# Kernel optimization log

Hardware: AMD Instinct MI355X
Metric: run time of the kernel (lower is better)

## Reference

```python
import jax, jax.numpy as jnp
import numpy as np

V = 50000
D = 128
EF = 16
E = 800000
LN_EPS = 1e-5


def setup_inputs() -> dict:
    key = jax.random.key(0)
    ks = jax.random.split(key, 9)
    h = jax.random.normal(ks[0], (V, D), dtype=jnp.float32)
    edge_index = jax.random.randint(ks[1], (2, E), 0, V, dtype=jnp.int64)
    edge_attr = jax.random.normal(ks[2], (E, EF), dtype=jnp.float32)
    # msg_mlp = Linear(D+EF, D) -> ReLU -> Dropout(0) -> Linear(D, D)
    s1 = 1.0 / np.sqrt(D + EF)
    s2 = 1.0 / np.sqrt(D)
    W1 = jax.random.uniform(ks[3], (D + EF, D), minval=-s1, maxval=s1, dtype=jnp.float32)
    b1 = jax.random.uniform(ks[4], (D,), minval=-s1, maxval=s1, dtype=jnp.float32)
    W2 = jax.random.uniform(ks[5], (D, D), minval=-s2, maxval=s2, dtype=jnp.float32)
    b2 = jax.random.uniform(ks[6], (D,), minval=-s2, maxval=s2, dtype=jnp.float32)
    gamma = jnp.ones((D,), dtype=jnp.float32)
    beta = jnp.zeros((D,), dtype=jnp.float32)
    return {"h": h, "edge_index": edge_index, "edge_attr": edge_attr,
            "W1": W1, "b1": b1, "W2": W2, "b2": b2,
            "gamma": gamma, "beta": beta}


def _layer_norm(x, gamma, beta):
    mu = jnp.mean(x, axis=-1, keepdims=True)
    var = jnp.mean(jnp.square(x - mu), axis=-1, keepdims=True)
    return (x - mu) * jax.lax.rsqrt(var + LN_EPS) * gamma + beta


def reference(h, edge_index, edge_attr, W1, b1, W2, b2, gamma, beta):
    src, dst = edge_index[0], edge_index[1]
    # gather source node features, concat edge features: [E, D+EF]
    x = jnp.concatenate([h[src], edge_attr], axis=-1)
    # per-edge message MLP (dropout p=0 -> identity)
    msg = jax.nn.relu(x @ W1 + b1) @ W2 + b2  # [E, D]
    # scatter-add messages to destinations
    agg = jax.ops.segment_sum(msg, dst, num_segments=V)  # [V, D]
    # count initialized to ones BEFORE scatter_add -> denominator = 1 + in_degree
    deg = jax.ops.segment_sum(jnp.ones((E,), dtype=h.dtype), dst, num_segments=V)
    count = (1.0 + deg)[:, None]  # [V, 1]
    return _layer_norm(h + agg / count, gamma, beta)
```

## Files before the change

kernel.cpp:

```cpp
#include <hip/hip_runtime.h>
#include <hip/hip_bf16.h>

#define V 50000
#define D 128
#define EF 16
#define E_EDGES 800000
#define NT 12500
#define USTR 136
#define XESTR 40
#define CSTR 136
#define NSCAN 196
#define EGRID 1024
#define UGRID 782

typedef __attribute__((ext_vector_type(8))) __bf16 bf16x8;
typedef __attribute__((ext_vector_type(4))) float f32x4;

__device__ inline unsigned short f2bf(float f) {
    unsigned u = __float_as_uint(f);
    u += 0x7FFF + ((u >> 16) & 1);
    return (unsigned short)(u >> 16);
}
__device__ inline unsigned pack2(float a, float b) {
    return (unsigned)f2bf(a) | ((unsigned)f2bf(b) << 16);
}
__device__ inline float bf2f(unsigned short u) {
    return __uint_as_float((unsigned)u << 16);
}

__global__ __launch_bounds__(256)
void setup_kernel(const int* __restrict__ ei, int* __restrict__ cnt,
                  float* __restrict__ agg,
                  const float* __restrict__ W1, const float* __restrict__ W2,
                  unsigned short* __restrict__ W1p, unsigned short* __restrict__ W2p) {
    int idx = blockIdx.x * 256 + threadIdx.x;
    *(float4*)(agg + ((size_t)idx << 2)) = (float4){0.f, 0.f, 0.f, 0.f};
    if (idx < E_EDGES) atomicAdd(&cnt[ei[E_EDGES + idx]], 1);
    if (idx < 5 * 128 * 32) {
        int kb = idx >> 12, rem = idx & 4095;
        int n = rem >> 5, kk = rem & 31;
        int k = kb * 32 + kk;
        W1p[idx] = f2bf((k < D + EF) ? W1[k * D + n] : 0.0f);
    }
    if (idx < 4 * 128 * 32) {
        int kb = idx >> 12, rem = idx & 4095;
        int n = rem >> 5, kk = rem & 31;
        W2p[idx] = f2bf(W2[(kb * 32 + kk) * D + n]);
    }
}

__global__ __launch_bounds__(256)
void u_gemm_kernel(const float* __restrict__ h,
                   const unsigned short* __restrict__ W1p,
                   unsigned short* __restrict__ U) {
    __shared__ __align__(16) unsigned short Hs[64 * USTR];
    const int tid  = threadIdx.x;
    const int lane = tid & 63;
    const int wave = tid >> 6;
    const int nlo  = lane & 15;
    const int kq   = lane >> 4;
    const int er   = tid >> 4;
    const int ec   = tid & 15;
    const int gbase = blockIdx.x << 6;

    bf16x8 B1[4][2];
    #pragma unroll
    for (int t = 0; t < 2; ++t) {
        int n = wave * 32 + t * 16 + nlo;
        #pragma unroll
        for (int kb = 0; kb < 4; ++kb)
            B1[kb][t] = *(const bf16x8*)(W1p + ((kb << 7) + n) * 32 + (kq << 3));
    }

    #pragma unroll
    for (int m = 0; m < 4; ++m) {
        int row = er + m * 16;
        int grow = gbase + row;
        unsigned* o = (unsigned*)(Hs + row * USTR + (ec << 3));
        if (grow < V) {
            const float4* p = (const float4*)(h + (size_t)grow * D + (ec << 3));
            float4 v0 = p[0], v1 = p[1];
            o[0] = pack2(v0.x, v0.y); o[1] = pack2(v0.z, v0.w);
            o[2] = pack2(v1.x, v1.y); o[3] = pack2(v1.z, v1.w);
        } else {
            o[0] = 0u; o[1] = 0u; o[2] = 0u; o[3] = 0u;
        }
    }
    __syncthreads();

    f32x4 acc[4][2];
    #pragma unroll
    for (int mt = 0; mt < 4; ++mt)
        #pragma unroll
        for (int t = 0; t < 2; ++t)
            acc[mt][t] = (f32x4){0.f, 0.f, 0.f, 0.f};

    #pragma unroll
    for (int kb = 0; kb < 4; ++kb) {
        bf16x8 A[4];
        int ko = kb * 32 + (kq << 3);
        #pragma unroll
        for (int mt = 0; mt < 4; ++mt)
            A[mt] = *(const bf16x8*)(Hs + (mt * 16 + nlo) * USTR + ko);
        #pragma unroll
        for (int mt = 0; mt < 4; ++mt)
            #pragma unroll
            for (int t = 0; t < 2; ++t)
                acc[mt][t] = __builtin_amdgcn_mfma_f32_16x16x32_bf16(A[mt], B1[kb][t], acc[mt][t], 0, 0, 0);
    }

    #pragma unroll
    for (int mt = 0; mt < 4; ++mt)
        #pragma unroll
        for (int t = 0; t < 2; ++t)
            #pragma unroll
            for (int r = 0; r < 4; ++r) {
                int row = mt * 16 + (kq << 2) + r;
                int grow = gbase + row;
                int col = wave * 32 + t * 16 + nlo;
                if (grow < V)
                    U[(size_t)grow * D + col] = f2bf(acc[mt][t][r]);
            }
}

__device__ inline int block_excl_scan(int x, int t, int* ws) {
    int lane = t & 63, w = t >> 6;
    int inc = x;
    #pragma unroll
    for (int off = 1; off < 64; off <<= 1) {
        int y = __shfl_up(inc, off);
        if (lane >= off) inc += y;
    }
    if (lane == 63) ws[w] = inc;
    __syncthreads();
    if (t == 0) {
        int r = 0;
        #pragma unroll
        for (int i = 0; i < 4; ++i) { int c = ws[i]; ws[i] = r; r += c; }
    }
    __syncthreads();
    return inc - x + ws[w];
}

__global__ __launch_bounds__(256)
void scan1_kernel(const int* __restrict__ cnt, int* __restrict__ cursor,
                  int* __restrict__ bsum) {
    __shared__ int ws[4];
    __shared__ int tot;
    int t = threadIdx.x;
    int i = blockIdx.x * 256 + t;
    int x = (i < V) ? cnt[i] : 0;
    int ex = block_excl_scan(x, t, ws);
    if (i < V) cursor[i] = ex;
    if (t == 255) tot = ex + x;
    __syncthreads();
    if (t == 0) bsum[blockIdx.x] = tot;
}

__global__ __launch_bounds__(256)
void scatter_kernel(const int* __restrict__ ei, int* __restrict__ cursor,
                    const int* __restrict__ bsum,
                    int* __restrict__ srcs, int* __restrict__ dsts,
                    int* __restrict__ eidx) {
    __shared__ int ws[4];
    __shared__ int sboff[NSCAN];
    int t = threadIdx.x;
    int x = (t < NSCAN) ? bsum[t] : 0;
    int ex = block_excl_scan(x, t, ws);
    if (t < NSCAN) sboff[t] = ex;
    __syncthreads();
    int e = blockIdx.x * 256 + t;
    int d = ei[E_EDGES + e];
    int pos = atomicAdd(&cursor[d], 1) + sboff[d >> 8];
    srcs[pos] = ei[e];
    dsts[pos] = d;
    eidx[pos] = e;
}

__global__ __launch_bounds__(256, 4)
void edge_kernel(const unsigned short* __restrict__ U,
                 const float* __restrict__ ea,
                 const int* __restrict__ srcs, const int* __restrict__ dsts,
                 const int* __restrict__ eidx,
                 const unsigned short* __restrict__ W1p, const unsigned short* __restrict__ W2p,
                 const float* __restrict__ b1, const float* __restrict__ b2,
                 float* __restrict__ agg) {
    __shared__ __align__(16) unsigned short Us[64 * USTR];
    __shared__ __align__(16) _Float16 Cs[64 * CSTR];
    __shared__ __align__(16) unsigned short Xe[64 * XESTR];
    __shared__ int sDst[2][64];

    const int tid  = threadIdx.x;
    const int lane = tid & 63;
    const int wave = tid >> 6;
    const int nlo  = lane & 15;
    const int kq   = lane >> 4;
    const int er   = tid >> 4;
    const int ec   = tid & 15;
    const int ee   = tid >> 2;
    const int eq   = tid & 3;

    bf16x8 B1e[2], B2[4][2];
    float b1v[2], b2v[2];
    #pragma unroll
    for (int t = 0; t < 2; ++t) {
        int n = wave * 32 + t * 16 + nlo;
        b1v[t] = b1[n];
        b2v[t] = b2[n];
        B1e[t] = *(const bf16x8*)(W1p + ((4 << 7) + n) * 32 + (kq << 3));
        #pragma unroll
        for (int kb = 0; kb < 4; ++kb)
            B2[kb][t] = *(const bf16x8*)(W2p + ((kb << 7) + n) * 32 + (kq << 3));
    }

    {
        unsigned* xz = (unsigned*)Xe;
        int i0 = tid, i1 = tid + 256;
        xz[(i0 >> 3) * (XESTR / 2) + 8 + (i0 & 7)] = 0u;
        xz[(i1 >> 3) * (XESTR / 2) + 8 + (i1 & 7)] = 0u;
    }

    const int base0 = blockIdx.x << 6;
    int a0 = srcs[base0 + er];
    int a1 = srcs[base0 + er + 16];
    int a2 = srcs[base0 + er + 32];
    int a3 = srcs[base0 + er + 48];
    int aev = eidx[base0 + ee];
    int ddcur = dsts[base0 + lane];
    bf16x8 pf0 = *(const bf16x8*)(U + (size_t)a0 * D + (ec << 3));
    bf16x8 pf1 = *(const bf16x8*)(U + (size_t)a1 * D + (ec << 3));
    bf16x8 pf2 = *(const bf16x8*)(U + (size_t)a2 * D + (ec << 3));
    bf16x8 pf3 = *(const bf16x8*)(U + (size_t)a3 * D + (ec << 3));
    float4 pfe = *(const float4*)(ea + (size_t)aev * EF + (eq << 2));

    int n1 = blockIdx.x + EGRID;
    int nb1 = (n1 < NT ? n1 : blockIdx.x) << 6;
    int i1s0 = srcs[nb1 + er];
    int i1s1 = srcs[nb1 + er + 16];
    int i1s2 = srcs[nb1 + er + 32];
    int i1s3 = srcs[nb1 + er + 48];
    int i1e  = eidx[nb1 + ee];
    int i1d  = dsts[nb1 + lane];

    int buf = 0;
    for (int tile = blockIdx.x; tile < NT; tile += EGRID) {
        if (tid < 64) sDst[buf][tid] = ddcur;
        *(bf16x8*)(Us + er * USTR + (ec << 3))        = pf0;
        *(bf16x8*)(Us + (er + 16) * USTR + (ec << 3)) = pf1;
        *(bf16x8*)(Us + (er + 32) * USTR + (ec << 3)) = pf2;
        *(bf16x8*)(Us + (er + 48) * USTR + (ec << 3)) = pf3;
        {
            unsigned* xp = (unsigned*)Xe + ee * (XESTR / 2) + (eq << 1);
            xp[0] = pack2(pfe.x, pfe.y);
            xp[1] = pack2(pfe.z, pfe.w);
        }
        __syncthreads();

        f32x4 accE[4][2];
        #pragma unroll
        for (int mt = 0; mt < 4; ++mt)
            #pragma unroll
            for (int t = 0; t < 2; ++t)
                #pragma unroll
                for (int r = 0; r < 4; ++r)
                    accE[mt][t][r] = bf2f(Us[(mt * 16 + (kq << 2) + r) * USTR + wave * 32 + t * 16 + nlo]);
        {
            bf16x8 A[4];
            #pragma unroll
            for (int mt = 0; mt < 4; ++mt)
                A[mt] = *(const bf16x8*)(Xe + (mt * 16 + nlo) * XESTR + (kq << 3));
            #pragma unroll
            for (int mt = 0; mt < 4; ++mt)
                #pragma unroll
                for (int t = 0; t < 2; ++t)
                    accE[mt][t] = __builtin_amdgcn_mfma_f32_16x16x32_bf16(A[mt], B1e[t], accE[mt][t], 0, 0, 0);
        }

        #pragma unroll
        for (int mt = 0; mt < 4; ++mt)
            #pragma unroll
            for (int t = 0; t < 2; ++t)
                #pragma unroll
                for (int r = 0; r < 4; ++r) {
                    int row = mt * 16 + (kq << 2) + r;
                    int col = wave * 32 + t * 16 + nlo;
                    Us[row * USTR + col] = f2bf(fmaxf(accE[mt][t][r] + b1v[t], 0.0f));
                }
        __syncthreads();

        f32x4 acc2[4][2];
        #pragma unroll
        for (int mt = 0; mt < 4; ++mt)
            #pragma unroll
            for (int t = 0; t < 2; ++t)
                acc2[mt][t] = (f32x4){0.f, 0.f, 0.f, 0.f};

        #pragma unroll
        for (int kb = 0; kb < 4; ++kb) {
            bf16x8 A[4];
            int ko = kb * 32 + (kq << 3);
            #pragma unroll
            for (int mt = 0; mt < 4; ++mt)
                A[mt] = *(const bf16x8*)(Us + (mt * 16 + nlo) * USTR + ko);
            #pragma unroll
            for (int mt = 0; mt < 4; ++mt)
                #pragma unroll
                for (int t = 0; t < 2; ++t)
                    acc2[mt][t] = __builtin_amdgcn_mfma_f32_16x16x32_bf16(A[mt], B2[kb][t], acc2[mt][t], 0, 0, 0);
        }

        #pragma unroll
        for (int mt = 0; mt < 4; ++mt)
            #pragma unroll
            for (int t = 0; t < 2; ++t)
                #pragma unroll
                for (int r = 0; r < 4; ++r) {
                    int row = mt * 16 + (kq << 2) + r;
                    int col = wave * 32 + t * 16 + nlo;
                    Cs[row * CSTR + col] = (_Float16)(acc2[mt][t][r] + b2v[t]);
                }
        __syncthreads();

        int n2 = tile + 2 * EGRID;
        int nb2 = (n2 < NT ? n2 : tile) << 6;
        int i2s0 = srcs[nb2 + er];
        int i2s1 = srcs[nb2 + er + 16];
        int i2s2 = srcs[nb2 + er + 32];
        int i2s3 = srcs[nb2 + er + 48];
        int i2e  = eidx[nb2 + ee];
        int i2d  = dsts[nb2 + lane];

        bf16x8 q0 = *(const bf16x8*)(U + (size_t)i1s0 * D + (ec << 3));
        bf16x8 q1 = *(const bf16x8*)(U + (size_t)i1s1 * D + (ec << 3));
        bf16x8 q2 = *(const bf16x8*)(U + (size_t)i1s2 * D + (ec << 3));
        bf16x8 q3 = *(const bf16x8*)(U + (size_t)i1s3 * D + (ec << 3));
        float4 qe = *(const float4*)(ea + (size_t)i1e * EF + (eq << 2));
        int nextdd = i1d;

        {
            int col = tid & 127;
            int rbase = (tid >> 7) << 5;
            float sum = 0.f;
            int cur = sDst[buf][rbase];
            for (int i = 0; i < 32; ++i) {
                int d = sDst[buf][rbase + i];
                if (d != cur) {
                    atomicAdd(&agg[(size_t)cur * D + col], sum);
                    sum = 0.f;
                    cur = d;
                }
                sum += (float)Cs[(rbase + i) * CSTR + col];
            }
            atomicAdd(&agg[(size_t)cur * D + col], sum);
        }

        pf0 = q0; pf1 = q1; pf2 = q2; pf3 = q3; pfe = qe; ddcur = nextdd;
        i1s0 = i2s0; i1s1 = i2s1; i1s2 = i2s2; i1s3 = i2s3; i1e = i2e; i1d = i2d;
        buf ^= 1;
    }
}

__global__ __launch_bounds__(256)
void finalize_kernel(const float* __restrict__ h, const float* __restrict__ agg,
                     const int* __restrict__ cnt,
                     const float* __restrict__ gamma, const float* __restrict__ beta,
                     float* __restrict__ out) {
    int wave = threadIdx.x >> 6, lane = threadIdx.x & 63;
    int v = blockIdx.x * 4 + wave;
    if (v >= V) return;
    float inv = 1.0f / (1.0f + (float)cnt[v]);
    const float* hr = h + (size_t)v * D;
    const float* ar = agg + (size_t)v * D;
    float x0 = hr[lane]      + ar[lane]      * inv;
    float x1 = hr[lane + 64] + ar[lane + 64] * inv;
    float s = x0 + x1;
    #pragma unroll
    for (int m = 32; m; m >>= 1) s += __shfl_xor(s, m);
    float mu = s * (1.0f / 128.0f);
    float d0 = x0 - mu, d1 = x1 - mu;
    float vs = d0 * d0 + d1 * d1;
    #pragma unroll
    for (int m = 32; m; m >>= 1) vs += __shfl_xor(vs, m);
    float rs = rsqrtf(vs * (1.0f / 128.0f) + 1e-5f);
    out[(size_t)v * D + lane]      = d0 * rs * gamma[lane]      + beta[lane];
    out[(size_t)v * D + 64 + lane] = d1 * rs * gamma[lane + 64] + beta[lane + 64];
}

extern "C" void kernel_launch(void* const* d_in, const int* in_sizes, int n_in,
                              void* d_out, int out_size, void* d_ws, size_t ws_size,
                              hipStream_t stream) {
    const float* h     = (const float*)d_in[0];
    const int*   ei    = (const int*)d_in[1];
    const float* ea    = (const float*)d_in[2];
    const float* W1    = (const float*)d_in[3];
    const float* b1    = (const float*)d_in[4];
    const float* W2    = (const float*)d_in[5];
    const float* b2    = (const float*)d_in[6];
    const float* gamma = (const float*)d_in[7];
    const float* beta  = (const float*)d_in[8];
    float* out = (float*)d_out;

    char* ws = (char*)d_ws;
    float*          agg    = (float*)ws;
    int*            cnt    = (int*)(ws + 25600000);
    int*            cursor = (int*)(ws + 25800000);
    int*            bsum   = (int*)(ws + 26000000);
    int*            srcs   = (int*)(ws + 26000800);
    int*            dsts   = (int*)(ws + 29200800);
    int*            eidx   = (int*)(ws + 32400800);
    unsigned short* W1p    = (unsigned short*)(ws + 35600800);
    unsigned short* W2p    = (unsigned short*)(ws + 35641760);
    unsigned short* U      = (unsigned short*)(ws + 35674528);

    hipMemsetAsync(cnt, 0, 200000, stream);
    setup_kernel<<<6250, 256, 0, stream>>>(ei, cnt, agg, W1, W2, W1p, W2p);
    u_gemm_kernel<<<UGRID, 256, 0, stream>>>(h, W1p, U);
    scan1_kernel<<<NSCAN, 256, 0, stream>>>(cnt, cursor, bsum);
    scatter_kernel<<<3125, 256, 0, stream>>>(ei, cursor, bsum, srcs, dsts, eidx);
    edge_kernel<<<EGRID, 256, 0, stream>>>(U, ea, srcs, dsts, eidx, W1p, W2p, b1, b2, agg);
    finalize_kernel<<<12500, 256, 0, stream>>>(h, agg, cnt, gamma, beta, out);
}
```

Measured before the change: 322.3 us.

## Use 512-thread edge blocks with one 16-column MFMA slice per wave

The edge kernel now launches 512 threads (8 waves) per block instead of 256. Each wave owns a single 16-column output slice rather than two, which halves the per-thread accumulators, weight fragments and gather loads, and the launch bounds target 6 blocks per CU. The persistent grid drops from 1024 to 768 blocks, and each thread's segmented scatter-add covers 16 rows instead of 32, which may raise the number of atomics to agg. The aim is more waves in flight to hide gather latency, at the cost of smaller MFMA work per wave and more block-level synchronisation overhead.

```diff
diff --git a/kernel.cpp b/kernel.cpp
--- a/kernel.cpp
+++ b/kernel.cpp
@@ -10,7 +10,7 @@
 #define XESTR 40
 #define CSTR 136
 #define NSCAN 196
-#define EGRID 1024
+#define EGRID 768
 #define UGRID 782
 
 typedef __attribute__((ext_vector_type(8))) __bf16 bf16x8;
@@ -177,7 +177,7 @@
     eidx[pos] = e;
 }
 
-__global__ __launch_bounds__(256, 4)
+__global__ __launch_bounds__(512, 6)
 void edge_kernel(const unsigned short* __restrict__ U,
                  const float* __restrict__ ea,
                  const int* __restrict__ srcs, const int* __restrict__ dsts,
@@ -197,73 +197,54 @@
     const int kq   = lane >> 4;
     const int er   = tid >> 4;
     const int ec   = tid & 15;
-    const int ee   = tid >> 2;
-    const int eq   = tid & 3;
-
-    bf16x8 B1e[2], B2[4][2];
-    float b1v[2], b2v[2];
-    #pragma unroll
-    for (int t = 0; t < 2; ++t) {
-        int n = wave * 32 + t * 16 + nlo;
-        b1v[t] = b1[n];
-        b2v[t] = b2[n];
-        B1e[t] = *(const bf16x8*)(W1p + ((4 << 7) + n) * 32 + (kq << 3));
-        #pragma unroll
-        for (int kb = 0; kb < 4; ++kb)
-            B2[kb][t] = *(const bf16x8*)(W2p + ((kb << 7) + n) * 32 + (kq << 3));
-    }
+    const int ee   = tid >> 3;
+    const int eq   = tid & 7;
+
+    bf16x8 B1e, B2[4];
+    float b1v, b2v;
+    const int ncol = wave * 16 + nlo;
+    b1v = b1[ncol];
+    b2v = b2[ncol];
+    B1e = *(const bf16x8*)(W1p + ((4 << 7) + ncol) * 32 + (kq << 3));
+    #pragma unroll
+    for (int kb = 0; kb < 4; ++kb)
+        B2[kb] = *(const bf16x8*)(W2p + ((kb << 7) + ncol) * 32 + (kq << 3));
 
     {
         unsigned* xz = (unsigned*)Xe;
-        int i0 = tid, i1 = tid + 256;
-        xz[(i0 >> 3) * (XESTR / 2) + 8 + (i0 & 7)] = 0u;
-        xz[(i1 >> 3) * (XESTR / 2) + 8 + (i1 & 7)] = 0u;
+        xz[(tid >> 3) * (XESTR / 2) + 8 + (tid & 7)] = 0u;
     }
 
     const int base0 = blockIdx.x << 6;
     int a0 = srcs[base0 + er];
-    int a1 = srcs[base0 + er + 16];
-    int a2 = srcs[base0 + er + 32];
-    int a3 = srcs[base0 + er + 48];
+    int a1 = srcs[base0 + er + 32];
     int aev = eidx[base0 + ee];
-    int ddcur = dsts[base0 + lane];
+    int ddcur = dsts[base0 + (tid & 63)];
     bf16x8 pf0 = *(const bf16x8*)(U + (size_t)a0 * D + (ec << 3));
     bf16x8 pf1 = *(const bf16x8*)(U + (size_t)a1 * D + (ec << 3));
-    bf16x8 pf2 = *(const bf16x8*)(U + (size_t)a2 * D + (ec << 3));
-    bf16x8 pf3 = *(const bf16x8*)(U + (size_t)a3 * D + (ec << 3));
-    float4 pfe = *(const float4*)(ea + (size_t)aev * EF + (eq << 2));
+    float2 pfe = *(const float2*)(ea + (size_t)aev * EF + (eq << 1));
 
     int n1 = blockIdx.x + EGRID;
     int nb1 = (n1 < NT ? n1 : blockIdx.x) << 6;
     int i1s0 = srcs[nb1 + er];
-    int i1s1 = srcs[nb1 + er + 16];
-    int i1s2 = srcs[nb1 + er + 32];
-    int i1s3 = srcs[nb1 + er + 48];
+    int i1s1 = srcs[nb1 + er + 32];
     int i1e  = eidx[nb1 + ee];
-    int i1d  = dsts[nb1 + lane];
+    int i1d  = dsts[nb1 + (tid & 63)];
 
     int buf = 0;
     for (int tile = blockIdx.x; tile < NT; tile += EGRID) {
         if (tid < 64) sDst[buf][tid] = ddcur;
         *(bf16x8*)(Us + er * USTR + (ec << 3))        = pf0;
-        *(bf16x8*)(Us + (er + 16) * USTR + (ec << 3)) = pf1;
-        *(bf16x8*)(Us + (er + 32) * USTR + (ec << 3)) = pf2;
-        *(bf16x8*)(Us + (er + 48) * USTR + (ec << 3)) = pf3;
-        {
-            unsigned* xp = (unsigned*)Xe + ee * (XESTR / 2) + (eq << 1);
-            xp[0] = pack2(pfe.x, pfe.y);
-            xp[1] = pack2(pfe.z, pfe.w);
-        }
+        *(bf16x8*)(Us + (er + 32) * USTR + (ec << 3)) = pf1;
+        ((unsigned*)Xe)[ee * (XESTR / 2) + eq] = pack2(pfe.x, pfe.y);
         __syncthreads();
 
-        f32x4 accE[4][2];
-        #pragma unroll
-        for (int mt = 0; mt < 4; ++mt)
-            #pragma unroll
-            for (int t = 0; t < 2; ++t)
-                #pragma unroll
-                for (int r = 0; r < 4; ++r)
-                    accE[mt][t][r] = bf2f(Us[(mt * 16 + (kq << 2) + r) * USTR + wave * 32 + t * 16 + nlo]);
+        f32x4 accE[4];
+        #pragma unroll
+        for (int mt = 0; mt < 4; ++mt)
+            #pragma unroll
+            for (int r = 0; r < 4; ++r)
+                accE[mt][r] = bf2f(Us[(mt * 16 + (kq << 2) + r) * USTR + ncol]);
         {
             bf16x8 A[4];
             #pragma unroll
@@ -271,29 +252,22 @@
                 A[mt] = *(const bf16x8*)(Xe + (mt * 16 + nlo) * XESTR + (kq << 3));
             #pragma unroll
             for (int mt = 0; mt < 4; ++mt)
-                #pragma unroll
-                for (int t = 0; t < 2; ++t)
-                    accE[mt][t] = __builtin_amdgcn_mfma_f32_16x16x32_bf16(A[mt], B1e[t], accE[mt][t], 0, 0, 0);
+                accE[mt] = __builtin_amdgcn_mfma_f32_16x16x32_bf16(A[mt], B1e, accE[mt], 0, 0, 0);
         }
 
         #pragma unroll
         for (int mt = 0; mt < 4; ++mt)
             #pragma unroll
-            for (int t = 0; t < 2; ++t)
-                #pragma unroll
-                for (int r = 0; r < 4; ++r) {
-                    int row = mt * 16 + (kq << 2) + r;
-                    int col = wave * 32 + t * 16 + nlo;
-                    Us[row * USTR + col] = f2bf(fmaxf(accE[mt][t][r] + b1v[t], 0.0f));
-                }
+            for (int r = 0; r < 4; ++r) {
+                int row = mt * 16 + (kq << 2) + r;
+                Us[row * USTR + ncol] = f2bf(fmaxf(accE[mt][r] + b1v, 0.0f));
+            }
         __syncthreads();
 
-        f32x4 acc2[4][2];
-        #pragma unroll
-        for (int mt = 0; mt < 4; ++mt)
-            #pragma unroll
-            for (int t = 0; t < 2; ++t)
-                acc2[mt][t] = (f32x4){0.f, 0.f, 0.f, 0.f};
+        f32x4 acc2[4];
+        #pragma unroll
+        for (int mt = 0; mt < 4; ++mt)
+            acc2[mt] = (f32x4){0.f, 0.f, 0.f, 0.f};
 
         #pragma unroll
         for (int kb = 0; kb < 4; ++kb) {
@@ -304,45 +278,37 @@
                 A[mt] = *(const bf16x8*)(Us + (mt * 16 + nlo) * USTR + ko);
             #pragma unroll
             for (int mt = 0; mt < 4; ++mt)
-                #pragma unroll
-                for (int t = 0; t < 2; ++t)
-                    acc2[mt][t] = __builtin_amdgcn_mfma_f32_16x16x32_bf16(A[mt], B2[kb][t], acc2[mt][t], 0, 0, 0);
+                acc2[mt] = __builtin_amdgcn_mfma_f32_16x16x32_bf16(A[mt], B2[kb], acc2[mt], 0, 0, 0);
         }
 
         #pragma unroll
         for (int mt = 0; mt < 4; ++mt)
             #pragma unroll
-            for (int t = 0; t < 2; ++t)
-                #pragma unroll
-                for (int r = 0; r < 4; ++r) {
-                    int row = mt * 16 + (kq << 2) + r;
-                    int col = wave * 32 + t * 16 + nlo;
-                    Cs[row * CSTR + col] = (_Float16)(acc2[mt][t][r] + b2v[t]);
-                }
+            for (int r = 0; r < 4; ++r) {
+                int row = mt * 16 + (kq << 2) + r;
+                Cs[row * CSTR + ncol] = (_Float16)(acc2[mt][r] + b2v);
+            }
         __syncthreads();
 
         int n2 = tile + 2 * EGRID;
         int nb2 = (n2 < NT ? n2 : tile) << 6;
         int i2s0 = srcs[nb2 + er];
-        int i2s1 = srcs[nb2 + er + 16];
-        int i2s2 = srcs[nb2 + er + 32];
-        int i2s3 = srcs[nb2 + er + 48];
+        int i2s1 = srcs[nb2 + er + 32];
         int i2e  = eidx[nb2 + ee];
-        int i2d  = dsts[nb2 + lane];
+        int i2d  = dsts[nb2 + (tid & 63)];
 
         bf16x8 q0 = *(const bf16x8*)(U + (size_t)i1s0 * D + (ec << 3));
         bf16x8 q1 = *(const bf16x8*)(U + (size_t)i1s1 * D + (ec << 3));
-        bf16x8 q2 = *(const bf16x8*)(U + (size_t)i1s2 * D + (ec << 3));
-        bf16x8 q3 = *(const bf16x8*)(U + (size_t)i1s3 * D + (ec << 3));
-        float4 qe = *(const float4*)(ea + (size_t)i1e * EF + (eq << 2));
+        float2 qe = *(const float2*)(ea + (size_t)i1e * EF + (eq << 1));
         int nextdd = i1d;
 
         {
             int col = tid & 127;
-            int rbase = (tid >> 7) << 5;
+            int rbase = (tid >> 7) << 4;
             float sum = 0.f;
             int cur = sDst[buf][rbase];
-            for (int i = 0; i < 32; ++i) {
+            #pragma unroll 4
+            for (int i = 0; i < 16; ++i) {
                 int d = sDst[buf][rbase + i];
                 if (d != cur) {
                     atomicAdd(&agg[(size_t)cur * D + col], sum);
@@ -354,8 +320,8 @@
             atomicAdd(&agg[(size_t)cur * D + col], sum);
         }
 
-        pf0 = q0; pf1 = q1; pf2 = q2; pf3 = q3; pfe = qe; ddcur = nextdd;
-        i1s0 = i2s0; i1s1 = i2s1; i1s2 = i2s2; i1s3 = i2s3; i1e = i2e; i1d = i2d;
+        pf0 = q0; pf1 = q1; pfe = qe; ddcur = nextdd;
+        i1s0 = i2s0; i1s1 = i2s1; i1e = i2e; i1d = i2d;
         buf ^= 1;
     }
 }
@@ -417,6 +383,6 @@
     u_gemm_kernel<<<UGRID, 256, 0, stream>>>(h, W1p, U);
     scan1_kernel<<<NSCAN, 256, 0, stream>>>(cnt, cursor, bsum);
     scatter_kernel<<<3125, 256, 0, stream>>>(ei, cursor, bsum, srcs, dsts, eidx);
-    edge_kernel<<<EGRID, 256, 0, stream>>>(U, ea, srcs, dsts, eidx, W1p, W2p, b1, b2, agg);
+    edge_kernel<<<EGRID, 512, 0, stream>>>(U, ea, srcs, dsts, eidx, W1p, W2p, b1, b2, agg);
     finalize_kernel<<<12500, 256, 0, stream>>>(h, agg, cnt, gamma, beta, out);
 }
```

Measured after the change: 327.9 us. Within noise of the previous version (+1.7%).

## Transpose MFMA operands for vectorized LDS epilogues and float4 scatter reduction

Applied to the files above, without the earlier changes.

Swaps the A/B operands of the MFMA calls so each lane holds four consecutive output columns, which lets the accumulator init, the bias+ReLU writeback and the fp16 output store use 64-bit packed LDS accesses instead of scalar 16-bit ones. Bias loads become float4, conversions use hardware packed bf16/fp16 converts, and the segmented scatter reduction now walks 8 rows with 4 columns per thread. The reduction emits four scalar atomics per flush over shorter row segments, so atomic traffic to agg may rise. The fp16 packing uses round-toward-zero, which changes rounding slightly.

```diff
diff --git a/kernel.cpp b/kernel.cpp
--- a/kernel.cpp
+++ b/kernel.cpp
@@ -15,6 +15,8 @@
 
 typedef __attribute__((ext_vector_type(8))) __bf16 bf16x8;
 typedef __attribute__((ext_vector_type(4))) float f32x4;
+typedef __attribute__((ext_vector_type(2))) __fp16 fp16x2;
+typedef __attribute__((ext_vector_type(2))) _Float16 f16x2;
 
 __device__ inline unsigned short f2bf(float f) {
     unsigned u = __float_as_uint(f);
@@ -26,6 +28,16 @@
 }
 __device__ inline float bf2f(unsigned short u) {
     return __uint_as_float((unsigned)u << 16);
+}
+__device__ inline unsigned pkbf(float a, float b) {
+    union { __hip_bfloat162 h; unsigned u; } v;
+    v.h = __float22bfloat162_rn(make_float2(a, b));
+    return v.u;
+}
+__device__ inline unsigned pkf16(float a, float b) {
+    union { fp16x2 h; unsigned u; } v;
+    v.h = __builtin_amdgcn_cvt_pkrtz(a, b);
+    return v.u;
 }
 
 __global__ __launch_bounds__(256)
@@ -201,12 +213,12 @@
     const int eq   = tid & 3;
 
     bf16x8 B1e[2], B2[4][2];
-    float b1v[2], b2v[2];
+    float4 b1n[2], b2n[2];
     #pragma unroll
     for (int t = 0; t < 2; ++t) {
         int n = wave * 32 + t * 16 + nlo;
-        b1v[t] = b1[n];
-        b2v[t] = b2[n];
+        b1n[t] = *(const float4*)(b1 + wave * 32 + t * 16 + (kq << 2));
+        b2n[t] = *(const float4*)(b2 + wave * 32 + t * 16 + (kq << 2));
         B1e[t] = *(const bf16x8*)(W1p + ((4 << 7) + n) * 32 + (kq << 3));
         #pragma unroll
         for (int kb = 0; kb < 4; ++kb)
@@ -251,8 +263,8 @@
         *(bf16x8*)(Us + (er + 48) * USTR + (ec << 3)) = pf3;
         {
             unsigned* xp = (unsigned*)Xe + ee * (XESTR / 2) + (eq << 1);
-            xp[0] = pack2(pfe.x, pfe.y);
-            xp[1] = pack2(pfe.z, pfe.w);
+            xp[0] = pkbf(pfe.x, pfe.y);
+            xp[1] = pkbf(pfe.z, pfe.w);
         }
         __syncthreads();
 
@@ -260,32 +272,36 @@
         #pragma unroll
         for (int mt = 0; mt < 4; ++mt)
             #pragma unroll
-            for (int t = 0; t < 2; ++t)
-                #pragma unroll
-                for (int r = 0; r < 4; ++r)
-                    accE[mt][t][r] = bf2f(Us[(mt * 16 + (kq << 2) + r) * USTR + wave * 32 + t * 16 + nlo]);
+            for (int t = 0; t < 2; ++t) {
+                uint2 uu = *(const uint2*)(Us + (mt * 16 + nlo) * USTR + wave * 32 + t * 16 + (kq << 2));
+                accE[mt][t][0] = bf2f((unsigned short)uu.x);
+                accE[mt][t][1] = bf2f((unsigned short)(uu.x >> 16));
+                accE[mt][t][2] = bf2f((unsigned short)uu.y);
+                accE[mt][t][3] = bf2f((unsigned short)(uu.y >> 16));
+            }
         {
-            bf16x8 A[4];
+            bf16x8 Xf[4];
             #pragma unroll
             for (int mt = 0; mt < 4; ++mt)
-                A[mt] = *(const bf16x8*)(Xe + (mt * 16 + nlo) * XESTR + (kq << 3));
+                Xf[mt] = *(const bf16x8*)(Xe + (mt * 16 + nlo) * XESTR + (kq << 3));
             #pragma unroll
             for (int mt = 0; mt < 4; ++mt)
                 #pragma unroll
                 for (int t = 0; t < 2; ++t)
-                    accE[mt][t] = __builtin_amdgcn_mfma_f32_16x16x32_bf16(A[mt], B1e[t], accE[mt][t], 0, 0, 0);
+                    accE[mt][t] = __builtin_amdgcn_mfma_f32_16x16x32_bf16(B1e[t], Xf[mt], accE[mt][t], 0, 0, 0);
         }
 
         #pragma unroll
         for (int mt = 0; mt < 4; ++mt)
             #pragma unroll
-            for (int t = 0; t < 2; ++t)
-                #pragma unroll
-                for (int r = 0; r < 4; ++r) {
-                    int row = mt * 16 + (kq << 2) + r;
-                    int col = wave * 32 + t * 16 + nlo;
-                    Us[row * USTR + col] = f2bf(fmaxf(accE[mt][t][r] + b1v[t], 0.0f));
-                }
+            for (int t = 0; t < 2; ++t) {
+                uint2 yw;
+                yw.x = pkbf(fmaxf(accE[mt][t][0] + b1n[t].x, 0.0f),
+                            fmaxf(accE[mt][t][1] + b1n[t].y, 0.0f));
+                yw.y = pkbf(fmaxf(accE[mt][t][2] + b1n[t].z, 0.0f),
+                            fmaxf(accE[mt][t][3] + b1n[t].w, 0.0f));
+                *(uint2*)(Us + (mt * 16 + nlo) * USTR + wave * 32 + t * 16 + (kq << 2)) = yw;
+            }
         __syncthreads();
 
         f32x4 acc2[4][2];
@@ -297,28 +313,27 @@
 
         #pragma unroll
         for (int kb = 0; kb < 4; ++kb) {
-            bf16x8 A[4];
+            bf16x8 Yf[4];
             int ko = kb * 32 + (kq << 3);
             #pragma unroll
             for (int mt = 0; mt < 4; ++mt)
-                A[mt] = *(const bf16x8*)(Us + (mt * 16 + nlo) * USTR + ko);
+                Yf[mt] = *(const bf16x8*)(Us + (mt * 16 + nlo) * USTR + ko);
             #pragma unroll
             for (int mt = 0; mt < 4; ++mt)
                 #pragma unroll
                 for (int t = 0; t < 2; ++t)
-                    acc2[mt][t] = __builtin_amdgcn_mfma_f32_16x16x32_bf16(A[mt], B2[kb][t], acc2[mt][t], 0, 0, 0);
+                    acc2[mt][t] = __builtin_amdgcn_mfma_f32_16x16x32_bf16(B2[kb][t], Yf[mt], acc2[mt][t], 0, 0, 0);
         }
 
         #pragma unroll
         for (int mt = 0; mt < 4; ++mt)
             #pragma unroll
-            for (int t = 0; t < 2; ++t)
-                #pragma unroll
-                for (int r = 0; r < 4; ++r) {
-                    int row = mt * 16 + (kq << 2) + r;
-                    int col = wave * 32 + t * 16 + nlo;
-                    Cs[row * CSTR + col] = (_Float16)(acc2[mt][t][r] + b2v[t]);
-                }
+            for (int t = 0; t < 2; ++t) {
+                uint2 cw;
+                cw.x = pkf16(acc2[mt][t][0] + b2n[t].x, acc2[mt][t][1] + b2n[t].y);
+                cw.y = pkf16(acc2[mt][t][2] + b2n[t].z, acc2[mt][t][3] + b2n[t].w);
+                *(uint2*)((unsigned short*)Cs + (size_t)(mt * 16 + nlo) * CSTR + wave * 32 + t * 16 + (kq << 2)) = cw;
+            }
         __syncthreads();
 
         int n2 = tile + 2 * EGRID;
@@ -338,20 +353,30 @@
         int nextdd = i1d;
 
         {
-            int col = tid & 127;
-            int rbase = (tid >> 7) << 5;
-            float sum = 0.f;
-            int cur = sDst[buf][rbase];
-            for (int i = 0; i < 32; ++i) {
-                int d = sDst[buf][rbase + i];
+            int q = tid & 31;
+            int mb = (tid >> 5) << 3;
+            float4 sum = {0.f, 0.f, 0.f, 0.f};
+            int cur = sDst[buf][mb];
+            #pragma unroll
+            for (int i = 0; i < 8; ++i) {
+                int m = mb + i;
+                int d = sDst[buf][m];
                 if (d != cur) {
-                    atomicAdd(&agg[(size_t)cur * D + col], sum);
-                    sum = 0.f;
+                    float* ap = agg + (size_t)cur * D + (q << 2);
+                    atomicAdd(ap + 0, sum.x); atomicAdd(ap + 1, sum.y);
+                    atomicAdd(ap + 2, sum.z); atomicAdd(ap + 3, sum.w);
+                    sum = (float4){0.f, 0.f, 0.f, 0.f};
                     cur = d;
                 }
-                sum += (float)Cs[(rbase + i) * CSTR + col];
+                uint2 cr = *(const uint2*)((const unsigned short*)Cs + (size_t)m * CSTR + (q << 2));
+                union { unsigned u; f16x2 h; } c0, c1;
+                c0.u = cr.x; c1.u = cr.y;
+                sum.x += (float)c0.h[0]; sum.y += (float)c0.h[1];
+                sum.z += (float)c1.h[0]; sum.w += (float)c1.h[1];
             }
-            atomicAdd(&agg[(size_t)cur * D + col], sum);
+            float* ap = agg + (size_t)cur * D + (q << 2);
+            atomicAdd(ap + 0, sum.x); atomicAdd(ap + 1, sum.y);
+            atomicAdd(ap + 2, sum.z); atomicAdd(ap + 3, sum.w);
         }
 
         pf0 = q0; pf1 = q1; pf2 = q2; pf3 = q3; pfe = qe; ddcur = nextdd;
@@ -412,7 +437,7 @@
     unsigned short* W2p    = (unsigned short*)(ws + 35641760);
     unsigned short* U      = (unsigned short*)(ws + 35674528);
 
-    hipMemsetAsync(cnt, 0, 200000, stream);
+    (void)hipMemsetAsync(cnt, 0, 200000, stream);
     setup_kernel<<<6250, 256, 0, stream>>>(ei, cnt, agg, W1, W2, W1p, W2p);
     u_gemm_kernel<<<UGRID, 256, 0, stream>>>(h, W1p, U);
     scan1_kernel<<<NSCAN, 256, 0, stream>>>(cnt, cursor, bsum);
```

Result: slower. 512.8 us (+59.1%).
